# Performance work log

Hardware: AMD Instinct MI355X
Metric: run time of the kernel (lower is better)

## Reference

```python
import jax, jax.numpy as jnp
import numpy as np

N_NODES = 50000
N_EDGES = 640000
D = 128
L = 3


def setup_inputs() -> dict:
    key = jax.random.key(0)
    k1, k2, k3, k4 = jax.random.split(key, 4)
    x = jax.random.normal(k1, (N_NODES, D), dtype=jnp.float32)
    # Glorot-ish scale so activations stay O(1) across 3 layers
    Ws = jax.random.normal(k2, (L, D, D), dtype=jnp.float32) * (1.0 / np.sqrt(D))
    bs = jnp.zeros((L, D), dtype=jnp.float32)
    edge_src = jax.random.randint(k3, (N_EDGES,), 0, N_NODES, dtype=jnp.int32)
    edge_dst = jax.random.randint(k4, (N_EDGES,), 0, N_NODES, dtype=jnp.int32)
    return {"x": x, "Ws": Ws, "bs": bs, "edge_src": edge_src, "edge_dst": edge_dst}


def reference(x, Ws, bs, edge_src, edge_dst):
    n = x.shape[0]
    ones = jnp.ones(edge_src.shape[0], dtype=x.dtype)
    # degrees, clamped to 1 as in dgl GraphConv(norm='both')
    deg_out = jnp.maximum(jax.ops.segment_sum(ones, edge_src, num_segments=n), 1.0)
    deg_in = jnp.maximum(jax.ops.segment_sum(ones, edge_dst, num_segments=n), 1.0)
    inv_sqrt_out = jax.lax.rsqrt(deg_out)[:, None]  # [N,1]
    inv_sqrt_in = jax.lax.rsqrt(deg_in)[:, None]    # [N,1]
    for l in range(Ws.shape[0]):
        h = x * inv_sqrt_out                         # src normalization
        msg = h[edge_src]                            # [E,D] gather
        agg = jax.ops.segment_sum(msg, edge_dst, num_segments=n)  # [N,D] scatter-add
        h = agg * inv_sqrt_in                        # dst normalization
        x = jax.nn.relu(h @ Ws[l] + bs[l])           # linear + ReLU
    return x
```

## Files before the change

### kernel.cpp

```cpp
#include <hip/hip_runtime.h>
#include <hip/hip_fp16.h>

typedef __attribute__((ext_vector_type(8))) _Float16 half8;
typedef __attribute__((ext_vector_type(4))) float f32x4;
typedef unsigned int u32;
typedef unsigned short u16;

#define ELL_PAD 64
#define NCHUNK 64
#define RSZ 8192


__global__ __launch_bounds__(256) void hist2(const int* __restrict__ esrc,
                                             const int* __restrict__ edst,
                                             u32* __restrict__ psrc,
                                             u32* __restrict__ pdst,
                                             const float* __restrict__ Ws,
                                             _Float16* __restrict__ Whi,
                                             _Float16* __restrict__ Wlo,
                                             int E, int N, int chunk, int R,
                                             int histBlocks, int packTotal) {
  __shared__ u32 bs_[RSZ];
  __shared__ u32 bd_[RSZ];
  if (blockIdx.x >= histBlocks) {
    int i = (blockIdx.x - histBlocks) * 256 + threadIdx.x;
    if (i < packTotal) {
      int lane  = i & 63;
      int kstep = (i >> 6) & 3;
      int ntile = (i >> 8) & 7;
      int layer = i >> 11;
      int n  = ntile * 16 + (lane & 15);
      int k0 = kstep * 32 + (lane >> 4) * 8;
      const float* W = Ws + (size_t)layer * 128 * 128;
      size_t base = (size_t)i * 8;
      for (int j = 0; j < 8; j++) {
        float v = W[(k0 + j) * 128 + n];
        _Float16 hi = (_Float16)v;
        Whi[base + j] = hi;
        Wlo[base + j] = (_Float16)(v - (float)hi);
      }
    }
    return;
  }
  int c = blockIdx.x / R;
  int r = blockIdx.x % R;
  int base = r * RSZ;
  int hi = min(RSZ, N - base);
  if (hi <= 0) return;
  for (int j = threadIdx.x; j < RSZ; j += 256) { bs_[j] = 0; bd_[j] = 0; }
  __syncthreads();
  int e0 = c * chunk;
  int e1 = min(E, e0 + chunk);
  for (int i = e0 + threadIdx.x; i < e1; i += 256) {
    unsigned ls = (unsigned)(esrc[i] - base);
    unsigned ld = (unsigned)(edst[i] - base);
    if (ls < (unsigned)RSZ) atomicAdd(&bs_[ls], 1u);
    if (ld < (unsigned)RSZ) atomicAdd(&bd_[ld], 1u);
  }
  __syncthreads();
  u32* ds = psrc + (size_t)c * N + base;
  u32* dd = pdst + (size_t)c * N + base;
  for (int j = threadIdx.x; j < hi; j += 256) { ds[j] = bs_[j]; dd[j] = bd_[j]; }
}


__global__ __launch_bounds__(256) void prep(const u32* __restrict__ psrc,
                                            u32* __restrict__ pdst,
                                            int* __restrict__ deg_out,
                                            int* __restrict__ deg_in, int N) {
  int i = blockIdx.x * 256 + threadIdx.x;
  if (i >= N) return;
  u32 s0 = 0, s1 = 0, s2 = 0, s3 = 0;
#pragma unroll
  for (int c = 0; c < NCHUNK; c += 4) {
    s0 += psrc[(size_t)(c + 0) * N + i];
    s1 += psrc[(size_t)(c + 1) * N + i];
    s2 += psrc[(size_t)(c + 2) * N + i];
    s3 += psrc[(size_t)(c + 3) * N + i];
  }
  deg_out[i] = (int)(s0 + s1 + s2 + s3);
  u32 cnt[NCHUNK];
#pragma unroll
  for (int c = 0; c < NCHUNK; c++) cnt[c] = pdst[(size_t)c * N + i];
  u32 run = (u32)i * ELL_PAD;
#pragma unroll
  for (int c = 0; c < NCHUNK; c++) { u32 t = cnt[c]; cnt[c] = run; run += t; }
#pragma unroll
  for (int c = 0; c < NCHUNK; c++) pdst[(size_t)c * N + i] = cnt[c];
  deg_in[i] = (int)(run - (u32)i * ELL_PAD);
}


__global__ __launch_bounds__(256) void xscale(const float* __restrict__ x,
                                              const int* __restrict__ deg_out,
                                              __half2* __restrict__ xh, int n64) {
  int gid = blockIdx.x * 256 + threadIdx.x;
  if (gid >= n64) return;
  int row = gid >> 6;
  int d = deg_out[row]; if (d < 1) d = 1;
  float s = rsqrtf((float)d);
  float2 v = ((const float2*)x)[gid];
  xh[gid] = __floats2half2_rn(v.x * s, v.y * s);
}


__global__ __launch_bounds__(256) void place(const int* __restrict__ esrc,
                                             const int* __restrict__ edst,
                                             const u32* __restrict__ pdst,
                                             u16* __restrict__ ell,
                                             int E, int N, int chunk, int R) {
  __shared__ u32 cur[RSZ];
  int c = blockIdx.x / R;
  int r = blockIdx.x % R;
  int base = r * RSZ;
  int hi = min(RSZ, N - base);
  if (hi <= 0) return;
  for (int j = threadIdx.x; j < hi; j += 256)
    cur[j] = pdst[(size_t)c * N + base + j];
  __syncthreads();
  int e0 = c * chunk;
  int e1 = min(E, e0 + chunk);
  for (int i = e0 + threadIdx.x; i < e1; i += 256) {
    int d = edst[i];
    unsigned loc = (unsigned)(d - base);
    if (loc < (unsigned)hi) {
      u32 p = atomicAdd(&cur[loc], 1u);
      u32 idx = p - (u32)d * ELL_PAD;
      if (idx < ELL_PAD) ell[p] = (u16)esrc[i];
    }
  }
}


__global__ __launch_bounds__(256) void spmm(const __half2* __restrict__ xh,
                                            const int* __restrict__ deg_in,
                                            const u16* __restrict__ ell,
                                            __half2* __restrict__ aggh,
                                            int npair, int n) {
  int pair = blockIdx.x * 4 + (threadIdx.x >> 6);
  if (pair >= npair) return;
  int lane = threadIdx.x & 63;
  int r0 = pair * 2, r1 = r0 + 1;
  int d0 = deg_in[r0];
  int d1 = (r1 < n) ? deg_in[r1] : 0;
  int l0 = d0 > ELL_PAD ? ELL_PAD : d0;
  int l1 = d1 > ELL_PAD ? ELL_PAD : d1;
  const u16* ep0 = ell + (size_t)r0 * ELL_PAD;
  const u16* ep1 = ell + (size_t)r1 * ELL_PAD;
  float ax0 = 0.f, ay0 = 0.f, ax1 = 0.f, ay1 = 0.f;

  int m = (l0 < l1 ? l0 : l1) & ~3;
  int e = 0;
  for (; e < m; e += 4) {
    ushort4 ia = *(const ushort4*)&ep0[e];
    ushort4 ib = *(const ushort4*)&ep1[e];
    __half2 a0 = xh[(size_t)ia.x * 64 + lane];
    __half2 a1 = xh[(size_t)ia.y * 64 + lane];
    __half2 a2 = xh[(size_t)ia.z * 64 + lane];
    __half2 a3 = xh[(size_t)ia.w * 64 + lane];
    __half2 b0 = xh[(size_t)ib.x * 64 + lane];
    __half2 b1 = xh[(size_t)ib.y * 64 + lane];
    __half2 b2 = xh[(size_t)ib.z * 64 + lane];
    __half2 b3 = xh[(size_t)ib.w * 64 + lane];
    float2 u0 = __half22float2(a0), u1 = __half22float2(a1);
    float2 u2 = __half22float2(a2), u3 = __half22float2(a3);
    float2 w0 = __half22float2(b0), w1 = __half22float2(b1);
    float2 w2 = __half22float2(b2), w3 = __half22float2(b3);
    ax0 += (u0.x + u1.x) + (u2.x + u3.x);
    ay0 += (u0.y + u1.y) + (u2.y + u3.y);
    ax1 += (w0.x + w1.x) + (w2.x + w3.x);
    ay1 += (w0.y + w1.y) + (w2.y + w3.y);
  }
  int e0i = e;
  for (; e0i + 4 <= l0; e0i += 4) {
    ushort4 ia = *(const ushort4*)&ep0[e0i];
    __half2 a0 = xh[(size_t)ia.x * 64 + lane];
    __half2 a1 = xh[(size_t)ia.y * 64 + lane];
    __half2 a2 = xh[(size_t)ia.z * 64 + lane];
    __half2 a3 = xh[(size_t)ia.w * 64 + lane];
    float2 u0 = __half22float2(a0), u1 = __half22float2(a1);
    float2 u2 = __half22float2(a2), u3 = __half22float2(a3);
    ax0 += (u0.x + u1.x) + (u2.x + u3.x);
    ay0 += (u0.y + u1.y) + (u2.y + u3.y);
  }
  for (; e0i < l0; e0i++) {
    float2 v = __half22float2(xh[(size_t)ep0[e0i] * 64 + lane]);
    ax0 += v.x; ay0 += v.y;
  }
  int e1i = e;
  for (; e1i + 4 <= l1; e1i += 4) {
    ushort4 ib = *(const ushort4*)&ep1[e1i];
    __half2 b0 = xh[(size_t)ib.x * 64 + lane];
    __half2 b1 = xh[(size_t)ib.y * 64 + lane];
    __half2 b2 = xh[(size_t)ib.z * 64 + lane];
    __half2 b3 = xh[(size_t)ib.w * 64 + lane];
    float2 w0 = __half22float2(b0), w1 = __half22float2(b1);
    float2 w2 = __half22float2(b2), w3 = __half22float2(b3);
    ax1 += (w0.x + w1.x) + (w2.x + w3.x);
    ay1 += (w0.y + w1.y) + (w2.y + w3.y);
  }
  for (; e1i < l1; e1i++) {
    float2 v = __half22float2(xh[(size_t)ep1[e1i] * 64 + lane]);
    ax1 += v.x; ay1 += v.y;
  }

  float si0 = rsqrtf((float)(d0 < 1 ? 1 : d0));
  ax0 *= si0; ay0 *= si0;
  aggh[(size_t)r0 * 64 + lane] = __floats2half2_rn(ax0, ay0);
  if (r1 < n) {
    float si1 = rsqrtf((float)(d1 < 1 ? 1 : d1));
    ax1 *= si1; ay1 *= si1;
    aggh[(size_t)r1 * 64 + lane] = __floats2half2_rn(ax1, ay1);
  }
}


__global__ __launch_bounds__(512) void gemm_mfma(const _Float16* __restrict__ A,
                                                 const _Float16* __restrict__ Whi,
                                                 const _Float16* __restrict__ Wlo,
                                                 const float* __restrict__ bias,
                                                 const int* __restrict__ deg_out,
                                                 __half* __restrict__ out16,
                                                 float* __restrict__ out32, int n) {
  __shared__ _Float16 Bh[16384];
  __shared__ _Float16 Bl[16384];
  {
    uint4* dh = (uint4*)Bh; const uint4* sh = (const uint4*)Whi;
    uint4* dl = (uint4*)Bl; const uint4* sl = (const uint4*)Wlo;
    for (int i = threadIdx.x; i < 2048; i += 512) { dh[i] = sh[i]; dl[i] = sl[i]; }
  }
  __syncthreads();

  const int wave = threadIdx.x >> 6;
  const int lane = threadIdx.x & 63;
  const int quad = lane >> 4;
  const int l16  = lane & 15;
  const int rowBase = blockIdx.x * 128 + wave * 16;
  const size_t arow = (size_t)(rowBase + l16) * 128;

  f32x4 acc[8];
#pragma unroll
  for (int nt = 0; nt < 8; nt++) acc[nt] = (f32x4){0.f, 0.f, 0.f, 0.f};

#pragma unroll
  for (int ks = 0; ks < 4; ks++) {
    half8 a = *(const half8*)&A[arow + ks * 32 + quad * 8];
#pragma unroll
    for (int nt = 0; nt < 8; nt++) {
      int boff = ((nt * 4 + ks) * 64 + lane) * 8;
      half8 bh = *(const half8*)&Bh[boff];
      half8 bl = *(const half8*)&Bl[boff];
      acc[nt] = __builtin_amdgcn_mfma_f32_16x16x32_f16(a, bh, acc[nt], 0, 0, 0);
      acc[nt] = __builtin_amdgcn_mfma_f32_16x16x32_f16(a, bl, acc[nt], 0, 0, 0);
    }
  }

  const int r0 = rowBase + quad * 4;
  float rs[4];
#pragma unroll
  for (int r = 0; r < 4; r++) {
    if (out16 && (r0 + r) < n) {
      int d = deg_out[r0 + r]; if (d < 1) d = 1;
      rs[r] = rsqrtf((float)d);
    } else rs[r] = 1.0f;
  }
#pragma unroll
  for (int nt = 0; nt < 8; nt++) {
    int col = nt * 16 + l16;
    float bv = bias[col];
#pragma unroll
    for (int r = 0; r < 4; r++) {
      int row = r0 + r;
      if (row < n) {
        float v = fmaxf(acc[nt][r] + bv, 0.f);
        if (out16) out16[(size_t)row * 128 + col] = __float2half(v * rs[r]);
        else       out32[(size_t)row * 128 + col] = v;
      }
    }
  }
}


extern "C" void kernel_launch(void* const* d_in, const int* in_sizes, int n_in,
                              void* d_out, int out_size, void* d_ws, size_t ws_size,
                              hipStream_t stream) {
  const float* x   = (const float*)d_in[0];
  const float* Ws  = (const float*)d_in[1];
  const float* bs  = (const float*)d_in[2];
  const int* esrc  = (const int*)d_in[3];
  const int* edst  = (const int*)d_in[4];

  const int D = 128;
  const int N = in_sizes[0] / D;
  const int E = in_sizes[3];
  const int L = in_sizes[1] / (D * D);
  const int Npad = ((N + 127) / 128) * 128;
  const int chunk = (E + NCHUNK - 1) / NCHUNK;
  const int R = (N + RSZ - 1) / RSZ;
  const int histBlocks = NCHUNK * R;
  const int packTotal = L * 2048;
  const int packBlocks = (packTotal + 255) / 256;

  char* base = (char*)d_ws;
  size_t off = 0;
  auto alloc = [&](size_t bytes) {
    char* p = base + off;
    off = (off + bytes + 255) & ~(size_t)255;
    return p;
  };
  int*      deg_out = (int*)alloc((size_t)N * 4);
  int*      deg_in  = (int*)alloc((size_t)N * 4);
  u16*      ell     = (u16*)alloc((size_t)N * ELL_PAD * 2);
  _Float16* Whi     = (_Float16*)alloc((size_t)L * 16384 * 2);
  _Float16* Wlo     = (_Float16*)alloc((size_t)L * 16384 * 2);
  _Float16* aggh    = (_Float16*)alloc((size_t)Npad * 128 * 2);
  _Float16* xh      = (_Float16*)alloc((size_t)Npad * 128 * 2);
  u32*      psrc    = (u32*)alloc((size_t)NCHUNK * N * 4);
  u32*      pdst    = (u32*)alloc((size_t)NCHUNK * N * 4);

  hist2<<<dim3(histBlocks + packBlocks), dim3(256), 0, stream>>>(
      esrc, edst, psrc, pdst, Ws, Whi, Wlo, E, N, chunk, R, histBlocks, packTotal);
  prep<<<dim3((N + 255) / 256), dim3(256), 0, stream>>>(psrc, pdst, deg_out, deg_in, N);
  xscale<<<dim3((N * 64 + 255) / 256), dim3(256), 0, stream>>>(
      x, deg_out, (__half2*)xh, N * 64);
  place<<<dim3(histBlocks), dim3(256), 0, stream>>>(
      esrc, edst, pdst, ell, E, N, chunk, R);

  float* outf = (float*)d_out;
  const int npair = (N + 1) / 2;
  const dim3 sgrid((npair + 3) / 4), sblk(256);
  const dim3 ggrid(Npad / 128), gblk(512);

  for (int l = 0; l < L; l++) {
    spmm<<<sgrid, sblk, 0, stream>>>((const __half2*)xh, deg_in, ell,
                                     (__half2*)aggh, npair, N);
    bool last = (l == L - 1);
    gemm_mfma<<<ggrid, gblk, 0, stream>>>(aggh,
                                          Whi + (size_t)l * 16384, Wlo + (size_t)l * 16384,
                                          bs + (size_t)l * D, deg_out,
                                          last ? nullptr : (__half*)xh,
                                          last ? outf : nullptr, N);
  }
}
```

Baseline: 272.7 us.

## Fuse SpMM aggregation and MFMA GEMM into one per-layer kernel

```diff
diff --git a/kernel.cpp b/kernel.cpp
--- a/kernel.cpp
+++ b/kernel.cpp
@@ -132,149 +132,119 @@
 }
 
 
-__global__ __launch_bounds__(256) void spmm(const __half2* __restrict__ xh,
-                                            const int* __restrict__ deg_in,
-                                            const u16* __restrict__ ell,
-                                            __half2* __restrict__ aggh,
-                                            int npair, int n) {
-  int pair = blockIdx.x * 4 + (threadIdx.x >> 6);
-  if (pair >= npair) return;
-  int lane = threadIdx.x & 63;
-  int r0 = pair * 2, r1 = r0 + 1;
-  int d0 = deg_in[r0];
-  int d1 = (r1 < n) ? deg_in[r1] : 0;
-  int l0 = d0 > ELL_PAD ? ELL_PAD : d0;
-  int l1 = d1 > ELL_PAD ? ELL_PAD : d1;
-  const u16* ep0 = ell + (size_t)r0 * ELL_PAD;
-  const u16* ep1 = ell + (size_t)r1 * ELL_PAD;
-  float ax0 = 0.f, ay0 = 0.f, ax1 = 0.f, ay1 = 0.f;
-
-  int m = (l0 < l1 ? l0 : l1) & ~3;
-  int e = 0;
-  for (; e < m; e += 4) {
-    ushort4 ia = *(const ushort4*)&ep0[e];
-    ushort4 ib = *(const ushort4*)&ep1[e];
-    __half2 a0 = xh[(size_t)ia.x * 64 + lane];
-    __half2 a1 = xh[(size_t)ia.y * 64 + lane];
-    __half2 a2 = xh[(size_t)ia.z * 64 + lane];
-    __half2 a3 = xh[(size_t)ia.w * 64 + lane];
-    __half2 b0 = xh[(size_t)ib.x * 64 + lane];
-    __half2 b1 = xh[(size_t)ib.y * 64 + lane];
-    __half2 b2 = xh[(size_t)ib.z * 64 + lane];
-    __half2 b3 = xh[(size_t)ib.w * 64 + lane];
-    float2 u0 = __half22float2(a0), u1 = __half22float2(a1);
-    float2 u2 = __half22float2(a2), u3 = __half22float2(a3);
-    float2 w0 = __half22float2(b0), w1 = __half22float2(b1);
-    float2 w2 = __half22float2(b2), w3 = __half22float2(b3);
-    ax0 += (u0.x + u1.x) + (u2.x + u3.x);
-    ay0 += (u0.y + u1.y) + (u2.y + u3.y);
-    ax1 += (w0.x + w1.x) + (w2.x + w3.x);
-    ay1 += (w0.y + w1.y) + (w2.y + w3.y);
-  }
-  int e0i = e;
-  for (; e0i + 4 <= l0; e0i += 4) {
-    ushort4 ia = *(const ushort4*)&ep0[e0i];
-    __half2 a0 = xh[(size_t)ia.x * 64 + lane];
-    __half2 a1 = xh[(size_t)ia.y * 64 + lane];
-    __half2 a2 = xh[(size_t)ia.z * 64 + lane];
-    __half2 a3 = xh[(size_t)ia.w * 64 + lane];
-    float2 u0 = __half22float2(a0), u1 = __half22float2(a1);
-    float2 u2 = __half22float2(a2), u3 = __half22float2(a3);
-    ax0 += (u0.x + u1.x) + (u2.x + u3.x);
-    ay0 += (u0.y + u1.y) + (u2.y + u3.y);
-  }
-  for (; e0i < l0; e0i++) {
-    float2 v = __half22float2(xh[(size_t)ep0[e0i] * 64 + lane]);
-    ax0 += v.x; ay0 += v.y;
-  }
-  int e1i = e;
-  for (; e1i + 4 <= l1; e1i += 4) {
-    ushort4 ib = *(const ushort4*)&ep1[e1i];
-    __half2 b0 = xh[(size_t)ib.x * 64 + lane];
-    __half2 b1 = xh[(size_t)ib.y * 64 + lane];
-    __half2 b2 = xh[(size_t)ib.z * 64 + lane];
-    __half2 b3 = xh[(size_t)ib.w * 64 + lane];
-    float2 w0 = __half22float2(b0), w1 = __half22float2(b1);
-    float2 w2 = __half22float2(b2), w3 = __half22float2(b3);
-    ax1 += (w0.x + w1.x) + (w2.x + w3.x);
-    ay1 += (w0.y + w1.y) + (w2.y + w3.y);
-  }
-  for (; e1i < l1; e1i++) {
-    float2 v = __half22float2(xh[(size_t)ep1[e1i] * 64 + lane]);
-    ax1 += v.x; ay1 += v.y;
-  }
-
-  float si0 = rsqrtf((float)(d0 < 1 ? 1 : d0));
-  ax0 *= si0; ay0 *= si0;
-  aggh[(size_t)r0 * 64 + lane] = __floats2half2_rn(ax0, ay0);
-  if (r1 < n) {
-    float si1 = rsqrtf((float)(d1 < 1 ? 1 : d1));
-    ax1 *= si1; ay1 *= si1;
-    aggh[(size_t)r1 * 64 + lane] = __floats2half2_rn(ax1, ay1);
-  }
-}
-
-
-__global__ __launch_bounds__(512) void gemm_mfma(const _Float16* __restrict__ A,
-                                                 const _Float16* __restrict__ Whi,
-                                                 const _Float16* __restrict__ Wlo,
-                                                 const float* __restrict__ bias,
-                                                 const int* __restrict__ deg_out,
-                                                 __half* __restrict__ out16,
-                                                 float* __restrict__ out32, int n) {
-  __shared__ _Float16 Bh[16384];
-  __shared__ _Float16 Bl[16384];
-  {
-    uint4* dh = (uint4*)Bh; const uint4* sh = (const uint4*)Whi;
-    uint4* dl = (uint4*)Bl; const uint4* sl = (const uint4*)Wlo;
-    for (int i = threadIdx.x; i < 2048; i += 512) { dh[i] = sh[i]; dl[i] = sl[i]; }
-  }
-  __syncthreads();
-
+__global__ __launch_bounds__(512) void layer16(const __half2* __restrict__ xh,
+                                               const int* __restrict__ deg_in,
+                                               const u16* __restrict__ ell,
+                                               const _Float16* __restrict__ Whi,
+                                               const _Float16* __restrict__ Wlo,
+                                               const float* __restrict__ bias,
+                                               const int* __restrict__ deg_out,
+                                               __half* __restrict__ out16,
+                                               float* __restrict__ out32, int n) {
+  __shared__ _Float16 As[16 * 136];
   const int wave = threadIdx.x >> 6;
   const int lane = threadIdx.x & 63;
+  const int rowBase = blockIdx.x * 16;
+
+  {
+    int r0 = rowBase + wave * 2, r1 = r0 + 1;
+    int d0 = (r0 < n) ? deg_in[r0] : 0;
+    int d1 = (r1 < n) ? deg_in[r1] : 0;
+    int l0 = d0 > ELL_PAD ? ELL_PAD : d0;
+    int l1 = d1 > ELL_PAD ? ELL_PAD : d1;
+    const u16* ep0 = ell + (size_t)(r0 < n ? r0 : 0) * ELL_PAD;
+    const u16* ep1 = ell + (size_t)(r1 < n ? r1 : 0) * ELL_PAD;
+    float ax0 = 0.f, ay0 = 0.f, ax1 = 0.f, ay1 = 0.f;
+
+    int m = (l0 < l1 ? l0 : l1) & ~3;
+    int e = 0;
+    for (; e < m; e += 4) {
+      ushort4 ia = *(const ushort4*)&ep0[e];
+      ushort4 ib = *(const ushort4*)&ep1[e];
+      __half2 a0 = xh[(size_t)ia.x * 64 + lane];
+      __half2 a1 = xh[(size_t)ia.y * 64 + lane];
+      __half2 a2 = xh[(size_t)ia.z * 64 + lane];
+      __half2 a3 = xh[(size_t)ia.w * 64 + lane];
+      __half2 b0 = xh[(size_t)ib.x * 64 + lane];
+      __half2 b1 = xh[(size_t)ib.y * 64 + lane];
+      __half2 b2 = xh[(size_t)ib.z * 64 + lane];
+      __half2 b3 = xh[(size_t)ib.w * 64 + lane];
+      float2 u0 = __half22float2(a0), u1 = __half22float2(a1);
+      float2 u2 = __half22float2(a2), u3 = __half22float2(a3);
+      float2 w0 = __half22float2(b0), w1 = __half22float2(b1);
+      float2 w2 = __half22float2(b2), w3 = __half22float2(b3);
+      ax0 += (u0.x + u1.x) + (u2.x + u3.x);
+      ay0 += (u0.y + u1.y) + (u2.y + u3.y);
+      ax1 += (w0.x + w1.x) + (w2.x + w3.x);
+      ay1 += (w0.y + w1.y) + (w2.y + w3.y);
+    }
+    int e0i = e;
+    for (; e0i + 4 <= l0; e0i += 4) {
+      ushort4 ia = *(const ushort4*)&ep0[e0i];
+      __half2 a0 = xh[(size_t)ia.x * 64 + lane];
+      __half2 a1 = xh[(size_t)ia.y * 64 + lane];
+      __half2 a2 = xh[(size_t)ia.z * 64 + lane];
+      __half2 a3 = xh[(size_t)ia.w * 64 + lane];
+      float2 u0 = __half22float2(a0), u1 = __half22float2(a1);
+      float2 u2 = __half22float2(a2), u3 = __half22float2(a3);
+      ax0 += (u0.x + u1.x) + (u2.x + u3.x);
+      ay0 += (u0.y + u1.y) + (u2.y + u3.y);
+    }
+    for (; e0i < l0; e0i++) {
+      float2 v = __half22float2(xh[(size_t)ep0[e0i] * 64 + lane]);
+      ax0 += v.x; ay0 += v.y;
+    }
+    int e1i = e;
+    for (; e1i + 4 <= l1; e1i += 4) {
+      ushort4 ib = *(const ushort4*)&ep1[e1i];
+      __half2 b0 = xh[(size_t)ib.x * 64 + lane];
+      __half2 b1 = xh[(size_t)ib.y * 64 + lane];
+      __half2 b2 = xh[(size_t)ib.z * 64 + lane];
+      __half2 b3 = xh[(size_t)ib.w * 64 + lane];
+      float2 w0 = __half22float2(b0), w1 = __half22float2(b1);
+      float2 w2 = __half22float2(b2), w3 = __half22float2(b3);
+      ax1 += (w0.x + w1.x) + (w2.x + w3.x);
+      ay1 += (w0.y + w1.y) + (w2.y + w3.y);
+    }
+    for (; e1i < l1; e1i++) {
+      float2 v = __half22float2(xh[(size_t)ep1[e1i] * 64 + lane]);
+      ax1 += v.x; ay1 += v.y;
+    }
+
+    float si0 = rsqrtf((float)(d0 < 1 ? 1 : d0));
+    float si1 = rsqrtf((float)(d1 < 1 ? 1 : d1));
+    *(__half2*)&As[(size_t)(wave * 2 + 0) * 136 + lane * 2] =
+        __floats2half2_rn(ax0 * si0, ay0 * si0);
+    *(__half2*)&As[(size_t)(wave * 2 + 1) * 136 + lane * 2] =
+        __floats2half2_rn(ax1 * si1, ay1 * si1);
+  }
+  __syncthreads();
+
   const int quad = lane >> 4;
   const int l16  = lane & 15;
-  const int rowBase = blockIdx.x * 128 + wave * 16;
-  const size_t arow = (size_t)(rowBase + l16) * 128;
-
-  f32x4 acc[8];
-#pragma unroll
-  for (int nt = 0; nt < 8; nt++) acc[nt] = (f32x4){0.f, 0.f, 0.f, 0.f};
-
+  f32x4 acc = (f32x4){0.f, 0.f, 0.f, 0.f};
 #pragma unroll
   for (int ks = 0; ks < 4; ks++) {
-    half8 a = *(const half8*)&A[arow + ks * 32 + quad * 8];
-#pragma unroll
-    for (int nt = 0; nt < 8; nt++) {
-      int boff = ((nt * 4 + ks) * 64 + lane) * 8;
-      half8 bh = *(const half8*)&Bh[boff];
-      half8 bl = *(const half8*)&Bl[boff];
-      acc[nt] = __builtin_amdgcn_mfma_f32_16x16x32_f16(a, bh, acc[nt], 0, 0, 0);
-      acc[nt] = __builtin_amdgcn_mfma_f32_16x16x32_f16(a, bl, acc[nt], 0, 0, 0);
-    }
+    half8 a = *(const half8*)&As[(size_t)l16 * 136 + ks * 32 + quad * 8];
+    half8 bh = *(const half8*)&Whi[((wave * 4 + ks) * 64 + lane) * 8];
+    half8 bl = *(const half8*)&Wlo[((wave * 4 + ks) * 64 + lane) * 8];
+    acc = __builtin_amdgcn_mfma_f32_16x16x32_f16(a, bh, acc, 0, 0, 0);
+    acc = __builtin_amdgcn_mfma_f32_16x16x32_f16(a, bl, acc, 0, 0, 0);
   }
 
   const int r0 = rowBase + quad * 4;
-  float rs[4];
+  const int col = wave * 16 + l16;
+  const float bv = bias[col];
 #pragma unroll
   for (int r = 0; r < 4; r++) {
-    if (out16 && (r0 + r) < n) {
-      int d = deg_out[r0 + r]; if (d < 1) d = 1;
-      rs[r] = rsqrtf((float)d);
-    } else rs[r] = 1.0f;
-  }
-#pragma unroll
-  for (int nt = 0; nt < 8; nt++) {
-    int col = nt * 16 + l16;
-    float bv = bias[col];
-#pragma unroll
-    for (int r = 0; r < 4; r++) {
-      int row = r0 + r;
-      if (row < n) {
-        float v = fmaxf(acc[nt][r] + bv, 0.f);
-        if (out16) out16[(size_t)row * 128 + col] = __float2half(v * rs[r]);
-        else       out32[(size_t)row * 128 + col] = v;
+    int row = r0 + r;
+    if (row < n) {
+      float v = fmaxf(acc[r] + bv, 0.f);
+      if (out16) {
+        int d = deg_out[row]; if (d < 1) d = 1;
+        out16[(size_t)row * 128 + col] = __float2half(v * rsqrtf((float)d));
+      } else {
+        out32[(size_t)row * 128 + col] = v;
       }
     }
   }
@@ -294,7 +264,7 @@
   const int N = in_sizes[0] / D;
   const int E = in_sizes[3];
   const int L = in_sizes[1] / (D * D);
-  const int Npad = ((N + 127) / 128) * 128;
+  const int Npad = ((N + 15) / 16) * 16;
   const int chunk = (E + NCHUNK - 1) / NCHUNK;
   const int R = (N + RSZ - 1) / RSZ;
   const int histBlocks = NCHUNK * R;
@@ -313,8 +283,8 @@
   u16*      ell     = (u16*)alloc((size_t)N * ELL_PAD * 2);
   _Float16* Whi     = (_Float16*)alloc((size_t)L * 16384 * 2);
   _Float16* Wlo     = (_Float16*)alloc((size_t)L * 16384 * 2);
-  _Float16* aggh    = (_Float16*)alloc((size_t)Npad * 128 * 2);
-  _Float16* xh      = (_Float16*)alloc((size_t)Npad * 128 * 2);
+  _Float16* xh0     = (_Float16*)alloc((size_t)Npad * 128 * 2);
+  _Float16* xh1     = (_Float16*)alloc((size_t)Npad * 128 * 2);
   u32*      psrc    = (u32*)alloc((size_t)NCHUNK * N * 4);
   u32*      pdst    = (u32*)alloc((size_t)NCHUNK * N * 4);
 
@@ -322,23 +292,21 @@
       esrc, edst, psrc, pdst, Ws, Whi, Wlo, E, N, chunk, R, histBlocks, packTotal);
   prep<<<dim3((N + 255) / 256), dim3(256), 0, stream>>>(psrc, pdst, deg_out, deg_in, N);
   xscale<<<dim3((N * 64 + 255) / 256), dim3(256), 0, stream>>>(
-      x, deg_out, (__half2*)xh, N * 64);
+      x, deg_out, (__half2*)xh0, N * 64);
   place<<<dim3(histBlocks), dim3(256), 0, stream>>>(
       esrc, edst, pdst, ell, E, N, chunk, R);
 
   float* outf = (float*)d_out;
-  const int npair = (N + 1) / 2;
-  const dim3 sgrid((npair + 3) / 4), sblk(256);
-  const dim3 ggrid(Npad / 128), gblk(512);
+  _Float16* ping[2] = {xh0, xh1};
+  const dim3 lgrid(Npad / 16), lblk(512);
 
   for (int l = 0; l < L; l++) {
-    spmm<<<sgrid, sblk, 0, stream>>>((const __half2*)xh, deg_in, ell,
-                                     (__half2*)aggh, npair, N);
     bool last = (l == L - 1);
-    gemm_mfma<<<ggrid, gblk, 0, stream>>>(aggh,
-                                          Whi + (size_t)l * 16384, Wlo + (size_t)l * 16384,
-                                          bs + (size_t)l * D, deg_out,
-                                          last ? nullptr : (__half*)xh,
-                                          last ? outf : nullptr, N);
-  }
-}
+    layer16<<<lgrid, lblk, 0, stream>>>(
+        (const __half2*)ping[l & 1], deg_in, ell,
+        Whi + (size_t)l * 16384, Wlo + (size_t)l * 16384,
+        bs + (size_t)l * D, deg_out,
+        last ? nullptr : (__half*)ping[(l + 1) & 1],
+        last ? outf : nullptr, N);
+  }
+}
```

After: 263.7 us. -3.3%, faster.
